# Kernel tuning notes

Hardware: AMD Instinct MI355X
Metric: run time of the kernel (lower is better)

## Reference

```python
import math
import jax, jax.numpy as jnp
import numpy as np

B, N, W, D, H = 16, 64, 128, 128, 4

def posenc(L, d):
    pos = jnp.arange(L, dtype=jnp.float32)[:, None]
    div = jnp.exp(jnp.arange(0, d, 2, dtype=jnp.float32) * (-math.log(10000.0) / d))
    pe = jnp.zeros((L, d), jnp.float32)
    pe = pe.at[:, 0::2].set(jnp.sin(pos * div))
    pe = pe.at[:, 1::2].set(jnp.cos(pos * div))
    return pe

def ln(x):
    # torch nn.LayerNorm(x.shape[1:]) created fresh each call: normalize over all non-batch dims, no affine
    ax = tuple(range(1, x.ndim))
    m = x.mean(ax, keepdims=True)
    v = ((x - m) ** 2).mean(ax, keepdims=True)
    return (x - m) / jnp.sqrt(v + 1e-5)

def conv1d(x, w, b):
    # x [B,C,L], w [Cout,Cin,K] (torch layout), VALID padding
    y = jax.lax.conv_general_dilated(x, w, (1,), 'VALID', dimension_numbers=('NCH', 'OIH', 'NCH'))
    return y + b[None, :, None]

def convt1d(x, w, b, stride, pad):
    # torch ConvTranspose1d, w [Cin,Cout,K]
    K = w.shape[2]
    w_ = jnp.flip(w, 2).transpose(1, 0, 2)  # [Cout,Cin,K]
    y = jax.lax.conv_general_dilated(x, w_, (1,), [(K - 1 - pad, K - 1 - pad)],
                                     lhs_dilation=(stride,), dimension_numbers=('NCH', 'OIH', 'NCH'))
    return y + b[None, :, None]

def mha(q, k, v, wi, bi, wo, bo):
    # torch nn.MultiheadAttention(batch_first=True), H heads
    d = q.shape[-1]
    qp = q @ wi[:d].T + bi[:d]
    kp = k @ wi[d:2 * d].T + bi[d:2 * d]
    vp = v @ wi[2 * d:].T + bi[2 * d:]
    def heads(t):
        b_, l_, _ = t.shape
        return t.reshape(b_, l_, H, d // H).transpose(0, 2, 1, 3)
    qh, kh, vh = heads(qp), heads(kp), heads(vp)
    s = jnp.einsum('bhqd,bhkd->bhqk', qh, kh) / jnp.sqrt(jnp.asarray(d // H, qh.dtype))
    o = jnp.einsum('bhqk,bhkd->bhqd', jax.nn.softmax(s, -1), vh)
    b_, l_ = q.shape[0], q.shape[1]
    return o.transpose(0, 2, 1, 3).reshape(b_, l_, d) @ wo.T + bo


def setup_inputs():
    key = jax.random.key(0)
    ks = iter(jax.random.split(key, 64))
    def w(shape, s=0.05):
        return jax.random.normal(next(ks), shape, jnp.float32) * s
    inp = {}
    inp['tokens'] = jax.random.randint(next(ks), (B, N, W), 0, 257, jnp.int32)
    inp['emb_table'] = w((257, D), 1.0)
    for nm in ['ce', 'ct', 'cg', 'ces', 'cts']:
        inp['w_' + nm] = w((D, D, 3))
        inp['b_' + nm] = w((D,))
    inp['mha_wi'] = w((3 * D, D)); inp['mha_bi'] = w((3 * D,))
    inp['mha_wo'] = w((D, D)); inp['mha_bo'] = w((D,))
    s = 1.0 / math.sqrt(D)
    inp['tgt1'] = jax.random.uniform(next(ks), (1, D), jnp.float32, -s, s)
    inp['tgt2'] = jax.random.uniform(next(ks), (1, D), jnp.float32, -s, s)
    for nm in ['mu', 'lv', 'di']:
        inp['w_' + nm] = w((D, D)); inp['b_' + nm] = w((D,))
    inp['eps'] = jax.random.normal(next(ks), (B, D), jnp.float32)
    inp['dk_w'] = w((32, 32)); inp['dk_b'] = w((32,))
    inp['dv_w'] = w((32, 32)); inp['dv_b'] = w((32,))
    inp['wt1'] = w((32, 64, 3)); inp['bt1'] = w((64,))
    inp['wt2'] = w((64, 128, 3)); inp['bt2'] = w((128,))
    for nm in ['sq', 'sk', 'sv']:
        inp[nm + '_w'] = w((128, 128)); inp[nm + '_b'] = w((128,))
    inp['wt3'] = w((128, 128, 3)); inp['bt3'] = w((128,))
    return inp


def reference(tokens, emb_table, w_ce, b_ce, w_ct, b_ct, w_cg, b_cg, w_ces, b_ces, w_cts, b_cts,
              mha_wi, mha_bi, mha_wo, mha_bo, tgt1, tgt2,
              w_mu, b_mu, w_lv, b_lv, w_di, b_di, eps,
              dk_w, dk_b, dv_w, dv_b, wt1, bt1, wt2, bt2,
              sq_w, sq_b, sk_w, sk_b, sv_w, sv_b, wt3, bt3):
    emb = emb_table[tokens] + posenc(W, D)                    # [B,N,W,D]
    flat = emb.reshape(B * N, W, D)                           # batch the per-sample torch loop

    def word_branch(wc, bc, act):
        h = act(conv1d(flat.transpose(0, 2, 1), wc, bc)).transpose(0, 2, 1)  # [BN,W-2,D]
        return mha(h, h, h, mha_wi, mha_bi, mha_wo, mha_bo)

    a_e = jax.nn.elu(word_branch(w_ce, b_ce, jax.nn.elu))
    a_t = jnp.tanh(word_branch(w_ct, b_ct, jnp.tanh))
    xw = ln((a_e * a_t).reshape(B, N, W - 2, D)).reshape(B * N, W - 2, D)

    h = jax.nn.elu(conv1d(xw.transpose(0, 2, 1), w_cg, b_cg)).transpose(0, 2, 1)  # [BN,W-4,D]
    q1 = jnp.broadcast_to(tgt1[None], (B * N, 1, D))
    out = mha(q1, h, h, mha_wi, mha_bi, mha_wo, mha_bo)[:, 0, :].reshape(B, N, D)

    se = out + posenc(N, D)                                   # sentence level

    def sent_branch(wc, bc, act):
        hh = act(conv1d(se.transpose(0, 2, 1), wc, bc)).transpose(0, 2, 1)       # [B,N-2,D]
        return mha(hh, hh, hh, mha_wi, mha_bi, mha_wo, mha_bo)

    s_e = jax.nn.elu(sent_branch(w_ces, b_ces, jax.nn.elu))
    s_t = jnp.tanh(sent_branch(w_cts, b_cts, jnp.tanh))
    xs = ln(s_e * s_t)
    q2 = jnp.broadcast_to(tgt2[None], (B, 1, D))
    doc = mha(q2, xs, xs, mha_wi, mha_bi, mha_wo, mha_bo)[:, 0, :]

    mu = doc @ w_mu.T + b_mu
    lv = doc @ w_lv.T + b_lv
    z = mu + eps * jnp.exp(0.5 * lv)

    h = (z @ w_di.T + b_di).reshape(B, 32, -1)                # [B,32,4]
    L = h.shape[2]
    k = jnp.einsum('oi,bil->bol', dk_w, h) + dk_b[None, :, None]
    v = jnp.einsum('oi,bil->bol', dv_w, h) + dv_b[None, :, None]
    kh = k.reshape(B, H, 8, L)
    vh = v.reshape(B, H, 8, L)
    att = jax.nn.softmax(jnp.einsum('bhdl,bhdm->bhlm', kh, vh) / jnp.sqrt(8.0), -1)
    h = jax.nn.elu(jnp.einsum('bhlm,bhdm->bhld', att, vh).reshape(B, 32, L))
    h = jax.nn.elu(ln(convt1d(h, wt1, bt1, 2, 1)))            # [B,64,7]
    h = jax.nn.elu(ln(convt1d(h, wt2, bt2, 2, 1)))            # [B,128,13]
    L2 = h.shape[2]
    qc = jnp.einsum('oi,bil->bol', sq_w, h) + sq_b[None, :, None]
    kc = jnp.einsum('oi,bil->bol', sk_w, h) + sk_b[None, :, None]
    vc = jnp.einsum('oi,bil->bol', sv_w, h) + sv_b[None, :, None]
    qh = qc.reshape(B, H, 32, L2)
    khh = kc.reshape(B, H, 32, L2)
    att = jax.nn.softmax(jnp.einsum('bhdl,bhdm->bhlm', qh, khh) / jnp.sqrt(32.0), -1)
    vr = vc.reshape(B, H, 32, L2).reshape(B, H, L2, 32)       # faithful torch .view reinterpretation
    h = jax.nn.elu(jnp.einsum('bhlm,bhmd->bhld', att, vr).reshape(B, 128, L2))
    recon = jax.nn.sigmoid(ln(convt1d(h, wt3, bt3, 1, 1)))    # [B,128,13]
    return recon, mu, lv
```

## Files before the change

kernel.cpp:

```cpp
#include <hip/hip_runtime.h>
#include <hip/hip_bf16.h>

typedef __hip_bfloat16 bf16;
typedef __attribute__((ext_vector_type(8))) short bf16x8;
typedef __attribute__((ext_vector_type(4))) float f32x4;

__device__ __forceinline__ float b2f(bf16 x){ return __bfloat162float(x); }
__device__ __forceinline__ bf16  f2b(float x){ return __float2bfloat16(x); }

#define LOG2E 1.4426950408889634f

__device__ __forceinline__ float fexp2(float x){
  float r; asm("v_exp_f32 %0, %1" : "=v"(r) : "v"(x)); return r;
}
__device__ __forceinline__ float fast_exp(float x){ return fexp2(x * LOG2E); }
__device__ __forceinline__ float eluf(float x){ return x > 0.f ? x : fast_exp(x) - 1.f; }
__device__ __forceinline__ float fast_tanh(float x){
  float cx = fminf(fmaxf(x, -15.f), 15.f);
  float t = fexp2(cx * (2.f*LOG2E));
  return (t - 1.f) / (t + 1.f);
}

#define PE_C (-0.07195578415606394f)

__device__ __forceinline__ float pe_val(int pos, int d){
  int j2 = d & ~1;
  float ang = (float)pos * expf((float)j2 * PE_C);
  return (d & 1) ? cosf(ang) : sinf(ang);
}

__device__ __forceinline__ void pack_one(const float* __restrict__ W, bf16* __restrict__ out,
                                         int K, int N, int conv, int t){
  int j = t & 7, lane = (t >> 3) & 63;
  int rest = t >> 9; int NT = N >> 4;
  int nt = rest % NT; int kb = rest / NT;
  int k = kb*32 + ((lane >> 4) << 3) + j;
  int n = nt*16 + (lane & 15);
  float v = conv ? W[n*384 + (k & 127)*3 + (k >> 7)] : W[(long)n*K + k];
  out[t] = f2b(v);
}

__global__ void k_prep(const float* __restrict__ w_ce, const float* __restrict__ w_ct,
                       const float* __restrict__ w_cg, const float* __restrict__ w_ces,
                       const float* __restrict__ w_cts, const float* __restrict__ wi,
                       const float* __restrict__ wo,
                       bf16* P_CE, bf16* P_CT, bf16* P_CG, bf16* P_CES, bf16* P_CTS,
                       bf16* P_WI, bf16* P_WO, float* __restrict__ pet){
  int bid = blockIdx.x;
  if (bid < 1152){
    int grp = bid / 192; int t = (bid % 192)*256 + threadIdx.x;
    const float* W; bf16* out; int K, N, conv;
    if      (grp == 0){ W = w_ce;  out = P_CE;  K=384; N=128; conv=1; }
    else if (grp == 1){ W = w_ct;  out = P_CT;  K=384; N=128; conv=1; }
    else if (grp == 2){ W = w_cg;  out = P_CG;  K=384; N=128; conv=1; }
    else if (grp == 3){ W = w_ces; out = P_CES; K=384; N=128; conv=1; }
    else if (grp == 4){ W = w_cts; out = P_CTS; K=384; N=128; conv=1; }
    else              { W = wi;    out = P_WI;  K=128; N=384; conv=0; }
    pack_one(W, out, K, N, conv, t);
  } else if (bid < 1216){
    int t = (bid - 1152)*256 + threadIdx.x;
    pack_one(wo, P_WO, 128, 128, 0, t);
  } else {
    int i = (bid - 1216)*256 + threadIdx.x;
    if (i < 16384) pet[i] = pe_val(i >> 7, i & 127);
  }
}

__global__ void k_qprep(const float* __restrict__ wi, const float* __restrict__ bi,
                        const float* __restrict__ t1, const float* __restrict__ t2,
                        float* __restrict__ rkv){
  int tid = threadIdx.x;
  __shared__ float qps[256];
  {
    int which = tid >> 7, jj = tid & 127;
    const float* t = which ? t2 : t1;
    float a = bi[jj];
    for (int i = 0; i < 128; ++i) a += wi[jj*128 + i] * t[i];
    qps[tid] = a;
  }
  __syncthreads();
  int i = tid & 127, which = tid >> 7;
  for (int h = 0; h < 4; ++h){
    float a = 0.f;
    for (int d = 0; d < 32; ++d) a += qps[which*128 + h*32 + d] * wi[(128 + h*32 + d)*128 + i];
    rkv[which*512 + h*128 + i] = a;
  }
}

__global__ void k_embed8(const int* __restrict__ tok, const float* __restrict__ tab,
                         const float* __restrict__ pet, bf16* __restrict__ out){
  int t = blockIdx.x*256 + threadIdx.x;
  int q = t & 15;
  int flat = t >> 4; int w = flat & 127;
  int tk = tok[flat];
  const float* ta = tab + tk*128 + q*8;
  const float* pe = pet + (w << 7) + q*8;
  bf16 ob[8];
  #pragma unroll
  for (int i = 0; i < 8; ++i) ob[i] = f2b(ta[i] + pe[i]);
  *(f32x4*)(out + (size_t)t*8) = *(f32x4*)ob;
}

__global__ void k_se(const bf16* __restrict__ in, const float* __restrict__ pet, bf16* __restrict__ out){
  int idx = blockIdx.x*256 + threadIdx.x;
  int d = idx & 127; int n = (idx >> 7) & 63;
  out[idx] = f2b(b2f(in[idx]) + pet[(n << 7) + d]);
}

__global__ __launch_bounds__(256)
void k_gemm_mfma(const bf16* __restrict__ A, const bf16* __restrict__ Bp,
                 const float* __restrict__ bias, bf16* __restrict__ C,
                 const bf16* __restrict__ mul,
                 int M, int K, int a_lout, int a_lind, int lda,
                 int NT, int n0t, int ldc, int act,
                 const float* __restrict__ lnst, int lngrp){
  __shared__ f32x4 AsV[2][512];
  char* As0 = (char*)AsV[0];
  char* As1 = (char*)AsV[1];
  int tid = threadIdx.x;
  int lane = tid & 63, wave = tid >> 6;
  int wm = wave >> 1, wn = wave & 1;
  int m0 = blockIdx.x*128;
  int by = blockIdx.y;

  long offA[2]; bool okA[2]; float lnm[2], lnr[2]; int sbyte[2];
  #pragma unroll
  for (int p = 0; p < 2; ++p){
    int e = tid + p*256;
    int row = e >> 2, kq = e & 3, m = m0 + row;
    okA[p] = (m < M);
    long off = 0;
    if (okA[p]){
      off = (a_lout > 0) ? (long)(m / a_lout)*a_lind + (long)(m % a_lout)*128 + kq*8
                         : (long)m*lda + kq*8;
    }
    offA[p] = off;
    lnm[p] = 0.f; lnr[p] = 1.f;
    if (lnst && okA[p]){ int g = (int)(off / (long)lngrp); lnm[p] = lnst[2*g]; lnr[p] = lnst[2*g+1]; }
    sbyte[p] = (row*64 + kq*16) ^ ((row & 7) << 4);
  }
  auto loadA = [&](int p, int kb)->float4{
    float4 v = make_float4(0.f,0.f,0.f,0.f);
    if (okA[p]){
      v = *(const float4*)(A + offA[p] + kb*32);
      if (lnst){
        bf16* pp = (bf16*)&v; bf16 oo[8];
        #pragma unroll
        for (int u = 0; u < 8; ++u) oo[u] = f2b((b2f(pp[u]) - lnm[p]) * lnr[p]);
        v = *(float4*)&oo[0];
      }
    }
    return v;
  };

  const bf16* bptr[4];
  size_t bstep = (size_t)NT*512;
  #pragma unroll
  for (int fn = 0; fn < 4; ++fn){
    int ntile = n0t + by*8 + wn*4 + fn;
    bptr[fn] = Bp + ((size_t)ntile*64 + lane)*8;
  }
  int abyte[4];
  #pragma unroll
  for (int fm = 0; fm < 4; ++fm){
    int row = wm*64 + fm*16 + (lane & 15);
    abyte[fm] = (row*64 + ((lane >> 4) << 4)) ^ ((row & 7) << 4);
  }

  f32x4 acc[4][4];
  #pragma unroll
  for (int i = 0; i < 4; ++i)
    #pragma unroll
    for (int j = 0; j < 4; ++j) acc[i][j] = (f32x4){0.f,0.f,0.f,0.f};

  float4 va0 = loadA(0, 0), va1 = loadA(1, 0);
  *(float4*)(As0 + sbyte[0]) = va0;
  *(float4*)(As0 + sbyte[1]) = va1;
  __syncthreads();

  int nk = K >> 5;
  for (int kb = 0; kb < nk; ++kb){
    char* cur = (kb & 1) ? As1 : As0;
    char* nxt = (kb & 1) ? As0 : As1;
    bool more = (kb + 1) < nk;
    if (more){ va0 = loadA(0, kb+1); va1 = loadA(1, kb+1); }
    bf16x8 bfr[4];
    #pragma unroll
    for (int fn = 0; fn < 4; ++fn) bfr[fn] = *(const bf16x8*)(bptr[fn] + (size_t)kb*bstep);
    bf16x8 afr[4];
    #pragma unroll
    for (int fm = 0; fm < 4; ++fm) afr[fm] = *(const bf16x8*)(cur + abyte[fm]);
    #pragma unroll
    for (int fm = 0; fm < 4; ++fm)
      #pragma unroll
      for (int fn = 0; fn < 4; ++fn)
        acc[fm][fn] = __builtin_amdgcn_mfma_f32_16x16x32_bf16(afr[fm], bfr[fn], acc[fm][fn], 0, 0, 0);
    if (more){
      *(float4*)(nxt + sbyte[0]) = va0;
      *(float4*)(nxt + sbyte[1]) = va1;
    }
    __syncthreads();
  }

  #pragma unroll
  for (int fm = 0; fm < 4; ++fm){
    #pragma unroll
    for (int r = 0; r < 4; ++r){
      int m = m0 + wm*64 + fm*16 + ((lane >> 4) << 2) + r;
      if (m >= M) continue;
      #pragma unroll
      for (int fn = 0; fn < 4; ++fn){
        int n = by*128 + wn*64 + fn*16 + (lane & 15);
        float v = acc[fm][fn][r] + (bias ? bias[n] : 0.f);
        if (act == 1) v = eluf(v);
        else if (act == 2) v = fast_tanh(v);
        if (mul) v *= b2f(mul[(long)m*ldc + n]);
        C[(long)m*ldc + n] = f2b(v);
      }
    }
  }
}

template<int L>
__global__ __launch_bounds__(256)
void k_attn_fused(const bf16* __restrict__ X, const bf16* __restrict__ Pwi,
                  const float* __restrict__ bi, bf16* __restrict__ o){
  constexpr int KB  = (L + 31) / 32;
  constexpr int MT  = KB * 2;
  constexpr int WMT = MT / 4;
  constexpr int NP  = KB * 32;
  constexpr int PRS = NP * 2;

  __shared__ alignas(16) char As[NP*256];
  __shared__ alignas(16) char Qb[NP*64];
  __shared__ alignas(16) char Kb[NP*64];
  __shared__ alignas(16) char Vt[32*PRS];
  char* Pb = As;

  int tid = threadIdx.x;
  int s = blockIdx.x >> 2, h = blockIdx.x & 3;
  const bf16* xb = X + (size_t)s*L*128;

  for (int e = tid; e < NP*16; e += 256){
    int row = e >> 4, c = e & 15;
    float4 v = make_float4(0.f,0.f,0.f,0.f);
    if (row < L) v = *(const float4*)(xb + (size_t)row*128 + c*8);
    *(float4*)(As + ((row*256 + c*16) ^ ((row & 7) << 4))) = v;
  }
  __syncthreads();

  int lane = tid & 63, wave = tid >> 6;
  const float qsc = 0.17677669529663687f * LOG2E;

  __builtin_amdgcn_s_setprio(1);
  #pragma unroll
  for (int mt = 0; mt < WMT; ++mt){
    int mtile = wave*WMT + mt;
    int arow = mtile*16 + (lane & 15);
    bf16x8 a4[4];
    #pragma unroll
    for (int kb = 0; kb < 4; ++kb)
      a4[kb] = *(const bf16x8*)(As + ((arow*256 + kb*64 + ((lane >> 4) << 4)) ^ ((arow & 7) << 4)));
    #pragma unroll
    for (int out = 0; out < 6; ++out){
      int which = out >> 1, nt = out & 1;
      int ntile = which*8 + h*2 + nt;
      f32x4 acc = (f32x4){0.f,0.f,0.f,0.f};
      #pragma unroll
      for (int kb = 0; kb < 4; ++kb){
        bf16x8 bfr = *(const bf16x8*)(Pwi + (((size_t)kb*24 + ntile)*64 + lane)*8);
        acc = __builtin_amdgcn_mfma_f32_16x16x32_bf16(a4[kb], bfr, acc, 0, 0, 0);
      }
      int col = lane & 15;
      float bia = bi[which*128 + h*32 + nt*16 + col];
      #pragma unroll
      for (int r = 0; r < 4; ++r){
        int row = mtile*16 + ((lane >> 4) << 2) + r;
        float outv = acc[r] + bia;
        if (which == 0){
          *(bf16*)(Qb + ((row*64 + (nt*16 + col)*2) ^ ((row & 7) << 4))) = f2b(outv * qsc);
        } else if (which == 1){
          *(bf16*)(Kb + ((row*64 + (nt*16 + col)*2) ^ ((row & 7) << 4))) = f2b(outv);
        } else {
          int d = nt*16 + col;
          *(bf16*)(Vt + ((d*PRS + row*2) ^ ((d & 7) << 4))) = f2b(outv);
        }
      }
    }
  }
  __builtin_amdgcn_s_setprio(0);
  __syncthreads();

  f32x4 acc[WMT][MT];
  #pragma unroll
  for (int mt = 0; mt < WMT; ++mt)
    #pragma unroll
    for (int nt = 0; nt < MT; ++nt) acc[mt][nt] = (f32x4){0.f,0.f,0.f,0.f};

  bf16x8 af[WMT];
  #pragma unroll
  for (int mt = 0; mt < WMT; ++mt){
    int row = (wave*WMT + mt)*16 + (lane & 15);
    af[mt] = *(const bf16x8*)(Qb + ((row*64 + ((lane >> 4) << 4)) ^ ((row & 7) << 4)));
  }
  __builtin_amdgcn_s_setprio(1);
  #pragma unroll
  for (int nt = 0; nt < MT; ++nt){
    int rk2 = nt*16 + (lane & 15);
    bf16x8 bfk = *(const bf16x8*)(Kb + ((rk2*64 + ((lane >> 4) << 4)) ^ ((rk2 & 7) << 4)));
    #pragma unroll
    for (int mt = 0; mt < WMT; ++mt)
      acc[mt][nt] = __builtin_amdgcn_mfma_f32_16x16x32_bf16(af[mt], bfk, acc[mt][nt], 0, 0, 0);
  }
  __builtin_amdgcn_s_setprio(0);

  const bool lastMask = (lane & 15) >= (L - (MT-1)*16);
  float pinv[WMT][4];
  #pragma unroll
  for (int mt = 0; mt < WMT; ++mt){
    #pragma unroll
    for (int r = 0; r < 4; ++r){
      float mx = -1e30f;
      #pragma unroll
      for (int nt = 0; nt < MT; ++nt){
        float v = acc[mt][nt][r];
        if (nt == MT-1 && lastMask){ v = -1e30f; acc[mt][nt][r] = v; }
        mx = fmaxf(mx, v);
      }
      mx = fmaxf(mx, __shfl_xor(mx, 1));
      mx = fmaxf(mx, __shfl_xor(mx, 2));
      mx = fmaxf(mx, __shfl_xor(mx, 4));
      mx = fmaxf(mx, __shfl_xor(mx, 8));
      float sum = 0.f;
      #pragma unroll
      for (int nt = 0; nt < MT; ++nt){
        float p = fexp2(acc[mt][nt][r] - mx);
        acc[mt][nt][r] = p;
        sum += p;
      }
      sum += __shfl_xor(sum, 1);
      sum += __shfl_xor(sum, 2);
      sum += __shfl_xor(sum, 4);
      sum += __shfl_xor(sum, 8);
      pinv[mt][r] = 1.f / sum;
      int row = (wave*WMT + mt)*16 + ((lane >> 4) << 2) + r;
      #pragma unroll
      for (int nt = 0; nt < MT; ++nt){
        int col = nt*16 + (lane & 15);
        *(bf16*)(Pb + ((row*PRS + col*2) ^ ((row & 7) << 4))) = f2b(acc[mt][nt][r]);
      }
    }
  }

  #pragma unroll
  for (int mt = 0; mt < WMT; ++mt){
    int mtile = wave*WMT + mt;
    f32x4 o0 = (f32x4){0.f,0.f,0.f,0.f}, o1 = (f32x4){0.f,0.f,0.f,0.f};
    __builtin_amdgcn_s_setprio(1);
    #pragma unroll
    for (int kb = 0; kb < KB; ++kb){
      int row = mtile*16 + (lane & 15);
      bf16x8 pa = *(const bf16x8*)(Pb + ((row*PRS + kb*64 + ((lane >> 4) << 4)) ^ ((row & 7) << 4)));
      int d0 = lane & 15;
      bf16x8 v0 = *(const bf16x8*)(Vt + ((d0*PRS + kb*64 + ((lane >> 4) << 4)) ^ ((d0 & 7) << 4)));
      bf16x8 v1 = *(const bf16x8*)(Vt + (((d0+16)*PRS + kb*64 + ((lane >> 4) << 4)) ^ (((d0+16) & 7) << 4)));
      o0 = __builtin_amdgcn_mfma_f32_16x16x32_bf16(pa, v0, o0, 0, 0, 0);
      o1 = __builtin_amdgcn_mfma_f32_16x16x32_bf16(pa, v1, o1, 0, 0, 0);
    }
    __builtin_amdgcn_s_setprio(0);
    #pragma unroll
    for (int r = 0; r < 4; ++r){
      int row = mtile*16 + ((lane >> 4) << 2) + r;
      if (row < L){
        size_t ob = ((size_t)s*L + row)*128 + h*32 + (lane & 15);
        o[ob]      = f2b(o0[r] * pinv[mt][r]);
        o[ob + 16] = f2b(o1[r] * pinv[mt][r]);
      }
    }
  }
}

template<int L>
__global__ __launch_bounds__(256)
void k_attn_tgt(const bf16* __restrict__ hin, const float* __restrict__ rk,
                const float* __restrict__ wi, const float* __restrict__ bi,
                bf16* __restrict__ outp){
  __shared__ alignas(16) char Hs[L*256];
  __shared__ float RKs[512];
  __shared__ float Ps[512];
  __shared__ float Cs[512];
  int tid = threadIdx.x, lane = tid & 63, wave = tid >> 6;
  int s = blockIdx.x;
  const bf16* hb = hin + (size_t)s*L*128;
  for (int e = tid; e < L*16; e += 256){
    int row = e >> 4, c = e & 15;
    *(float4*)(Hs + row*256 + ((c ^ (row & 7)) << 4)) = *(const float4*)(hb + row*128 + c*8);
  }
  for (int e = tid; e < 512; e += 256) RKs[e] = rk[e];
  __syncthreads();

  int j0 = lane, j1 = lane + 64;
  float v0 = -1e30f, v1 = -1e30f;
  if (j0 < L){
    float a = 0.f;
    #pragma unroll
    for (int c = 0; c < 16; ++c){
      bf16x8 x = *(const bf16x8*)(Hs + j0*256 + ((c ^ (j0 & 7)) << 4));
      #pragma unroll
      for (int u = 0; u < 8; ++u) a += b2f(((bf16*)&x)[u]) * RKs[wave*128 + c*8 + u];
    }
    v0 = a * 0.17677669529663687f;
  }
  if (j1 < L){
    float a = 0.f;
    #pragma unroll
    for (int c = 0; c < 16; ++c){
      bf16x8 x = *(const bf16x8*)(Hs + j1*256 + ((c ^ (j1 & 7)) << 4));
      #pragma unroll
      for (int u = 0; u < 8; ++u) a += b2f(((bf16*)&x)[u]) * RKs[wave*128 + c*8 + u];
    }
    v1 = a * 0.17677669529663687f;
  }
  float mx = fmaxf(v0, v1);
  #pragma unroll
  for (int off = 32; off; off >>= 1) mx = fmaxf(mx, __shfl_xor(mx, off));
  float e0 = (j0 < L) ? fast_exp(v0 - mx) : 0.f;
  float e1 = (j1 < L) ? fast_exp(v1 - mx) : 0.f;
  float sum = e0 + e1;
  #pragma unroll
  for (int off = 32; off; off >>= 1) sum += __shfl_xor(sum, off);
  float inv = 1.f / sum;
  Ps[wave*128 + j0] = e0 * inv;
  Ps[wave*128 + j1] = e1 * inv;

  int i0 = lane*2;
  float c0 = 0.f, c1 = 0.f;
  for (int j = 0; j < L; ++j){
    float p = Ps[wave*128 + j];
    short2 w2 = *(const short2*)(Hs + j*256 + (((i0 >> 3) ^ (j & 7)) << 4) + (i0 & 7)*2);
    c0 += p * b2f(*(bf16*)&w2.x);
    c1 += p * b2f(*(bf16*)&w2.y);
  }
  Cs[wave*128 + i0]     = c0;
  Cs[wave*128 + i0 + 1] = c1;
  __syncthreads();

  if (tid < 128){
    int h2 = tid >> 5;
    float a = bi[256 + tid];
    const float* wr = wi + (size_t)(256 + tid)*128;
    for (int i = 0; i < 128; ++i) a += wr[i] * Cs[h2*128 + i];
    outp[(size_t)s*128 + tid] = f2b(a);
  }
}

__global__ void k_ln_partial(const bf16* __restrict__ x, float* __restrict__ part, int GS, int P){
  int pi = blockIdx.x % P;
  int chunk8 = GS / P / 8;
  size_t base = (size_t)(blockIdx.x / P)*GS + (size_t)pi*(GS/P);
  float s = 0.f, s2 = 0.f;
  for (int i = threadIdx.x; i < chunk8; i += 256){
    f32x4 raw = *(const f32x4*)(x + base + (size_t)i*8);
    const bf16* xb = (const bf16*)&raw;
    #pragma unroll
    for (int j = 0; j < 8; ++j){ float v = b2f(xb[j]); s += v; s2 += v*v; }
  }
  #pragma unroll
  for (int off = 32; off; off >>= 1){ s += __shfl_xor(s, off); s2 += __shfl_xor(s2, off); }
  __shared__ float sh[8];
  int lane = threadIdx.x & 63, wv = threadIdx.x >> 6;
  if (lane == 0){ sh[wv] = s; sh[4 + wv] = s2; }
  __syncthreads();
  if (threadIdx.x == 0){
    part[blockIdx.x*2]     = sh[0]+sh[1]+sh[2]+sh[3];
    part[blockIdx.x*2 + 1] = sh[4]+sh[5]+sh[6]+sh[7];
  }
}

__global__ void k_ln_fin(const float* __restrict__ part, float* __restrict__ stats, int P, int GS){
  int g = blockIdx.x;
  float s = 0.f, s2 = 0.f;
  for (int i = threadIdx.x; i < P; i += 256){ s += part[(g*P + i)*2]; s2 += part[(g*P + i)*2 + 1]; }
  #pragma unroll
  for (int off = 32; off; off >>= 1){ s += __shfl_xor(s, off); s2 += __shfl_xor(s2, off); }
  __shared__ float sh[8];
  int lane = threadIdx.x & 63, wv = threadIdx.x >> 6;
  if (lane == 0){ sh[wv] = s; sh[4 + wv] = s2; }
  __syncthreads();
  if (threadIdx.x == 0){
    float S = sh[0]+sh[1]+sh[2]+sh[3], S2 = sh[4]+sh[5]+sh[6]+sh[7];
    float mean = S / GS;
    float var = S2 / GS - mean*mean;
    stats[g*2] = mean; stats[g*2 + 1] = rsqrtf(var + 1e-5f);
  }
}

__global__ void k_ln_small_bf16(const bf16* __restrict__ x, bf16* __restrict__ y, int n){
  int g = blockIdx.x;
  const bf16* xb = x + (size_t)g*n;
  bf16* yb = y + (size_t)g*n;
  float s = 0.f, s2 = 0.f;
  for (int i = threadIdx.x; i < n; i += 256){ float v = b2f(xb[i]); s += v; s2 += v*v; }
  #pragma unroll
  for (int off = 32; off; off >>= 1){ s += __shfl_xor(s, off); s2 += __shfl_xor(s2, off); }
  __shared__ float sh[8];  __shared__ float ms[2];
  int lane = threadIdx.x & 63, wv = threadIdx.x >> 6;
  if (lane == 0){ sh[wv] = s; sh[4 + wv] = s2; }
  __syncthreads();
  if (threadIdx.x == 0){
    float S = sh[0]+sh[1]+sh[2]+sh[3], S2 = sh[4]+sh[5]+sh[6]+sh[7];
    float mean = S / n;
    ms[0] = mean; ms[1] = rsqrtf(S2 / n - mean*mean + 1e-5f);
  }
  __syncthreads();
  float mean = ms[0], inv = ms[1];
  for (int i = threadIdx.x; i < n; i += 256) yb[i] = f2b((b2f(xb[i]) - mean)*inv);
}

__global__ void k_ln_small_f32(const float* __restrict__ x, float* __restrict__ y, int n, int act){
  int g = blockIdx.x;
  const float* xb = x + (size_t)g*n;
  float* yb = y + (size_t)g*n;
  float s = 0.f, s2 = 0.f;
  for (int i = threadIdx.x; i < n; i += 256){ float v = xb[i]; s += v; s2 += v*v; }
  #pragma unroll
  for (int off = 32; off; off >>= 1){ s += __shfl_xor(s, off); s2 += __shfl_xor(s2, off); }
  __shared__ float sh[8];  __shared__ float ms[2];
  int lane = threadIdx.x & 63, wv = threadIdx.x >> 6;
  if (lane == 0){ sh[wv] = s; sh[4 + wv] = s2; }
  __syncthreads();
  if (threadIdx.x == 0){
    float S = sh[0]+sh[1]+sh[2]+sh[3], S2 = sh[4]+sh[5]+sh[6]+sh[7];
    float mean = S / n;
    ms[0] = mean; ms[1] = rsqrtf(S2 / n - mean*mean + 1e-5f);
  }
  __syncthreads();
  float mean = ms[0], inv = ms[1];
  for (int i = threadIdx.x; i < n; i += 256){
    float v = (xb[i] - mean)*inv;
    if (act == 1) v = eluf(v);
    else if (act == 3) v = 1.f/(1.f + fast_exp(-v));
    yb[i] = v;
  }
}

__global__ void k_muz(const bf16* __restrict__ doc, const float* __restrict__ w_mu, const float* __restrict__ b_mu,
                      const float* __restrict__ w_lv, const float* __restrict__ b_lv,
                      const float* __restrict__ eps, float* __restrict__ mu_out, float* __restrict__ lv_out,
                      float* __restrict__ z){
  int t = blockIdx.x*256 + threadIdx.x;
  if (t >= 2048) return;
  int b = t >> 7, j = t & 127;
  const bf16* dr = doc + b*128;
  float mu = b_mu[j], lv = b_lv[j];
  for (int i = 0; i < 128; ++i){
    float x = b2f(dr[i]);
    mu += x * w_mu[j*128 + i];
    lv += x * w_lv[j*128 + i];
  }
  mu_out[t] = mu; lv_out[t] = lv;
  z[t] = mu + eps[t] * fast_exp(0.5f * lv);
}

__global__ void k_vecmat(const float* __restrict__ x, const float* __restrict__ w,
                         const float* __restrict__ bias, float* __restrict__ y){
  int t = blockIdx.x*256 + threadIdx.x;
  if (t >= 2048) return;
  int b = t >> 7, j = t & 127;
  float a = bias[j];
  const float* xb = x + b*128;
  for (int i = 0; i < 128; ++i) a += xb[i] * w[j*128 + i];
  y[t] = a;
}

__global__ void k_chanproj2(const float* __restrict__ x,
                            const float* __restrict__ w1, const float* __restrict__ b1,
                            const float* __restrict__ w2, const float* __restrict__ b2,
                            float* __restrict__ y1, float* __restrict__ y2,
                            int Bn, int C, int L){
  int idx = blockIdx.x*256 + threadIdx.x;
  if (idx >= Bn*C*L) return;
  int l = idx % L; int t2 = idx / L; int o = t2 % C; int b = t2 / C;
  float a1 = b1[o], a2 = b2[o];
  const float* xb = x + (size_t)b*C*L + l;
  for (int i = 0; i < C; ++i){
    float xv = xb[i*L];
    a1 += w1[(size_t)o*C + i]*xv;
    a2 += w2[(size_t)o*C + i]*xv;
  }
  y1[idx] = a1; y2[idx] = a2;
}

__global__ void k_chanproj3(const float* __restrict__ x,
                            const float* __restrict__ w1, const float* __restrict__ b1,
                            const float* __restrict__ w2, const float* __restrict__ b2,
                            const float* __restrict__ w3, const float* __restrict__ b3,
                            float* __restrict__ y1, float* __restrict__ y2, float* __restrict__ y3,
                            int Bn, int C, int L){
  int idx = blockIdx.x*256 + threadIdx.x;
  if (idx >= Bn*C*L) return;
  int l = idx % L; int t2 = idx / L; int o = t2 % C; int b = t2 / C;
  float a1 = b1[o], a2 = b2[o], a3 = b3[o];
  const float* xb = x + (size_t)b*C*L + l;
  for (int i = 0; i < C; ++i){
    float xv = xb[i*L];
    a1 += w1[(size_t)o*C + i]*xv;
    a2 += w2[(size_t)o*C + i]*xv;
    a3 += w3[(size_t)o*C + i]*xv;
  }
  y1[idx] = a1; y2[idx] = a2; y3[idx] = a3;
}

__global__ __launch_bounds__(128)
void k_dec_attn1(const float* __restrict__ kd, const float* __restrict__ vd, float* __restrict__ out){
  int b = blockIdx.x, tid = threadIdx.x;
  __shared__ float ksh[128], vsh[128], sc[64];
  ksh[tid] = kd[b*128 + tid]; vsh[tid] = vd[b*128 + tid];
  __syncthreads();
  if (tid < 64){
    int h = tid >> 4, l = (tid >> 2) & 3, m = tid & 3;
    float a = 0.f;
    #pragma unroll
    for (int d = 0; d < 8; ++d) a += ksh[(h*8 + d)*4 + l] * vsh[(h*8 + d)*4 + m];
    sc[tid] = a * 0.35355339059327373f;
  }
  __syncthreads();
  if (tid < 16){
    int base = tid*4;
    float mx = fmaxf(fmaxf(sc[base], sc[base+1]), fmaxf(sc[base+2], sc[base+3]));
    float e0 = fast_exp(sc[base]-mx), e1 = fast_exp(sc[base+1]-mx), e2 = fast_exp(sc[base+2]-mx), e3 = fast_exp(sc[base+3]-mx);
    float inv = 1.f/(e0+e1+e2+e3);
    sc[base] = e0*inv; sc[base+1] = e1*inv; sc[base+2] = e2*inv; sc[base+3] = e3*inv;
  }
  __syncthreads();
  {
    int h = tid >> 5, rem = tid & 31, l = rem >> 3, d = rem & 7;
    float a = 0.f;
    #pragma unroll
    for (int m = 0; m < 4; ++m) a += sc[h*16 + l*4 + m] * vsh[(h*8 + d)*4 + m];
    out[b*128 + tid] = eluf(a);
  }
}

__global__ __launch_bounds__(256)
void k_dec_attn2(const float* __restrict__ qc, const float* __restrict__ kc,
                 const float* __restrict__ vc, float* __restrict__ out){
  int b = blockIdx.x >> 2, h = blockIdx.x & 3, tid = threadIdx.x;
  __shared__ float sc[169];
  const float* qb = qc + b*1664 + h*416;
  const float* kb = kc + b*1664 + h*416;
  const float* vb = vc + b*1664 + h*416;
  if (tid < 169){
    int l = tid/13, m = tid - l*13;
    float a = 0.f;
    #pragma unroll
    for (int d = 0; d < 32; ++d) a += qb[d*13 + l] * kb[d*13 + m];
    sc[tid] = a * 0.17677669529663687f;
  }
  __syncthreads();
  if (tid < 13){
    float mx = -1e30f;
    for (int m = 0; m < 13; ++m) mx = fmaxf(mx, sc[tid*13 + m]);
    float s = 0.f;
    for (int m = 0; m < 13; ++m){ float p = fast_exp(sc[tid*13 + m] - mx); sc[tid*13 + m] = p; s += p; }
    float inv = 1.f/s;
    for (int m = 0; m < 13; ++m) sc[tid*13 + m] *= inv;
  }
  __syncthreads();
  for (int idx = tid; idx < 416; idx += 256){
    int l = idx >> 5, d = idx & 31;
    float a = 0.f;
    for (int m = 0; m < 13; ++m) a += sc[l*13 + m] * vb[m*32 + d];
    out[b*1664 + h*416 + idx] = eluf(a);
  }
}

__global__ __launch_bounds__(256)
void k_convt(const float* __restrict__ x, const float* __restrict__ w,
             const float* __restrict__ bias, float* __restrict__ y,
             int Bn, int Ci, int Co, int Lin, int Lout, int stride, int pad, int nch){
  __shared__ float xs[1664];
  int b = blockIdx.x / nch;
  int c0 = (blockIdx.x % nch)*16;
  int tid = threadIdx.x;
  for (int i = tid; i < Ci*Lin; i += 256) xs[i] = x[(size_t)b*Ci*Lin + i];
  __syncthreads();
  int co = c0 + (tid & 15);
  int lo = tid >> 4;
  if (co >= Co || lo >= Lout) return;
  float a = bias[co];
  for (int k = 0; k < 3; ++k){
    int t = lo + pad - k;
    if (t < 0 || (t % stride)) continue;
    int li = t / stride;
    if (li >= Lin) continue;
    float aa = 0.f;
    for (int ci = 0; ci < Ci; ++ci) aa += xs[ci*Lin + li] * w[(size_t)ci*Co*3 + co*3 + k];
    a += aa;
  }
  y[(size_t)b*Co*Lout + co*Lout + lo] = a;
}

extern "C" void kernel_launch(void* const* d_in, const int* in_sizes, int n_in,
                              void* d_out, int out_size, void* d_ws, size_t ws_size,
                              hipStream_t stream){
  const int*   tokens = (const int*)  d_in[0];
  const float* tab    = (const float*)d_in[1];
  const float* w_ce = (const float*)d_in[2];  const float* b_ce = (const float*)d_in[3];
  const float* w_ct = (const float*)d_in[4];  const float* b_ct = (const float*)d_in[5];
  const float* w_cg = (const float*)d_in[6];  const float* b_cg = (const float*)d_in[7];
  const float* w_ces= (const float*)d_in[8];  const float* b_ces= (const float*)d_in[9];
  const float* w_cts= (const float*)d_in[10]; const float* b_cts= (const float*)d_in[11];
  const float* wi   = (const float*)d_in[12]; const float* bi   = (const float*)d_in[13];
  const float* wo   = (const float*)d_in[14]; const float* bo   = (const float*)d_in[15];
  const float* tgt1 = (const float*)d_in[16]; const float* tgt2 = (const float*)d_in[17];
  const float* w_mu = (const float*)d_in[18]; const float* b_mu = (const float*)d_in[19];
  const float* w_lv = (const float*)d_in[20]; const float* b_lv = (const float*)d_in[21];
  const float* w_di = (const float*)d_in[22]; const float* b_di = (const float*)d_in[23];
  const float* epsb = (const float*)d_in[24];
  const float* dk_w = (const float*)d_in[25]; const float* dk_b = (const float*)d_in[26];
  const float* dv_w = (const float*)d_in[27]; const float* dv_b = (const float*)d_in[28];
  const float* wt1  = (const float*)d_in[29]; const float* bt1  = (const float*)d_in[30];
  const float* wt2  = (const float*)d_in[31]; const float* bt2  = (const float*)d_in[32];
  const float* sq_w = (const float*)d_in[33]; const float* sq_b = (const float*)d_in[34];
  const float* sk_w = (const float*)d_in[35]; const float* sk_b = (const float*)d_in[36];
  const float* sv_w = (const float*)d_in[37]; const float* sv_b = (const float*)d_in[38];
  const float* wt3  = (const float*)d_in[39]; const float* bt3  = (const float*)d_in[40];

  float* dout = (float*)d_out;

  char* ws = (char*)d_ws;
  size_t off = 0;
  auto take = [&](size_t bytes)->char*{ char* p = ws + off; off += (bytes + 255) & ~(size_t)255; return p; };
  bf16* EMB  = (bf16*)take(16777216ull*2);
  bf16* HB   = (bf16*)take(16515072ull*2);
  bf16* OB   = (bf16*)take(16515072ull*2);
  bf16* AE   = (bf16*)take(16515072ull*2);
  bf16* O1   = (bf16*)take(131072ull*2);
  bf16* OUTB = (bf16*)take(131072ull*2);
  bf16* SEB  = (bf16*)take(131072ull*2);
  bf16* SH   = (bf16*)take(126976ull*2);
  bf16* SCT  = (bf16*)take(126976ull*2);
  bf16* SO   = (bf16*)take(126976ull*2);
  bf16* SAE  = (bf16*)take(126976ull*2);
  bf16* XS   = (bf16*)take(126976ull*2);
  bf16* DO1  = (bf16*)take(2048ull*2);
  bf16* DOC  = (bf16*)take(2048ull*2);
  float* RK  = (float*)take(1024*4);
  float* PART= (float*)take(2016ull*2*4);
  float* STATS=(float*)take(32*4);
  float* Z   = (float*)take(2048*4);
  float* H3  = (float*)take(2048*4);
  float* KD  = (float*)take(2048*4);
  float* VD  = (float*)take(2048*4);
  float* DEC1= (float*)take(2048*4);
  float* C1  = (float*)take(7168*4);
  float* DEC2= (float*)take(7168*4);
  float* C2  = (float*)take(26624*4);
  float* DEC3= (float*)take(26624*4);
  float* QC  = (float*)take(26624*4);
  float* KC  = (float*)take(26624*4);
  float* VC  = (float*)take(26624*4);
  float* DEC4= (float*)take(26624*4);
  float* C3  = (float*)take(26624*4);
  float* PET = (float*)take(16384*4);
  bf16* P_CE = (bf16*)take(49152ull*2);
  bf16* P_CT = (bf16*)take(49152ull*2);
  bf16* P_CG = (bf16*)take(49152ull*2);
  bf16* P_CES= (bf16*)take(49152ull*2);
  bf16* P_CTS= (bf16*)take(49152ull*2);
  bf16* P_WI = (bf16*)take(49152ull*2);
  bf16* P_WO = (bf16*)take(16384ull*2);
  (void)ws_size; (void)in_sizes; (void)n_in; (void)out_size;

  auto cdiv = [](long a, long b){ return (int)((a + b - 1)/b); };
  auto gemm = [&](const bf16* A, const bf16* Bpp, const float* bias, bf16* C, const bf16* mul,
                  int M, int N, int K, int a_lout, int a_lind, int lda, int NT, int n0t, int ldc, int act,
                  const float* lnst, int lngrp){
    dim3 g(cdiv(M,128), N/128);
    k_gemm_mfma<<<g, 256, 0, stream>>>(A, Bpp, bias, C, mul,
                                       M, K, a_lout, a_lind, lda, NT, n0t, ldc, act, lnst, lngrp);
  };

  k_prep<<<1280, 256, 0, stream>>>(w_ce, w_ct, w_cg, w_ces, w_cts, wi, wo,
                                   P_CE, P_CT, P_CG, P_CES, P_CTS, P_WI, P_WO, PET);
  k_qprep<<<1, 256, 0, stream>>>(wi, bi, tgt1, tgt2, RK);
  k_embed8<<<8192, 256, 0, stream>>>(tokens, tab, PET, EMB);

  gemm(EMB, P_CE, b_ce, HB, nullptr, 129024, 128, 384, 126, 16384, 0, 8, 0, 128, 1, nullptr, 0);
  gemm(EMB, P_CT, b_ct, OB, nullptr, 129024, 128, 384, 126, 16384, 0, 8, 0, 128, 2, nullptr, 0);

  k_attn_fused<126><<<4096, 256, 0, stream>>>(HB, P_WI, bi, EMB);
  gemm(EMB, P_WO, bo, AE, nullptr, 129024, 128, 128, 0, 0, 128, 8, 0, 128, 1, nullptr, 0);

  k_attn_fused<126><<<4096, 256, 0, stream>>>(OB, P_WI, bi, EMB);
  gemm(EMB, P_WO, bo, HB, AE, 129024, 128, 128, 0, 0, 128, 8, 0, 128, 2, nullptr, 0);

  k_ln_partial<<<2016, 256, 0, stream>>>(HB, PART, 1032192, 126);
  k_ln_fin<<<16, 256, 0, stream>>>(PART, STATS, 126, 1032192);

  gemm(HB, P_CG, b_cg, OB, nullptr, 126976, 128, 384, 124, 16128, 0, 8, 0, 128, 1, STATS, 1032192);

  k_attn_tgt<124><<<1024, 256, 0, stream>>>(OB, RK, wi, bi, O1);
  gemm(O1, P_WO, bo, OUTB, nullptr, 1024, 128, 128, 0, 0, 128, 8, 0, 128, 0, nullptr, 0);

  k_se<<<512, 256, 0, stream>>>(OUTB, PET, SEB);

  gemm(SEB, P_CES, b_ces, SH, nullptr, 992, 128, 384, 62, 8192, 0, 8, 0, 128, 1, nullptr, 0);
  gemm(SEB, P_CTS, b_cts, SCT, nullptr, 992, 128, 384, 62, 8192, 0, 8, 0, 128, 2, nullptr, 0);

  k_attn_fused<62><<<64, 256, 0, stream>>>(SH, P_WI, bi, SO);
  gemm(SO, P_WO, bo, SAE, nullptr, 992, 128, 128, 0, 0, 128, 8, 0, 128, 1, nullptr, 0);

  k_attn_fused<62><<<64, 256, 0, stream>>>(SCT, P_WI, bi, SO);
  gemm(SO, P_WO, bo, SH, SAE, 992, 128, 128, 0, 0, 128, 8, 0, 128, 2, nullptr, 0);

  k_ln_small_bf16<<<16, 256, 0, stream>>>(SH, XS, 7936);

  k_attn_tgt<62><<<16, 256, 0, stream>>>(XS, RK + 512, wi, bi, DO1);
  gemm(DO1, P_WO, bo, DOC, nullptr, 16, 128, 128, 0, 0, 128, 8, 0, 128, 0, nullptr, 0);

  k_muz<<<8, 256, 0, stream>>>(DOC, w_mu, b_mu, w_lv, b_lv, epsb, dout + 26624, dout + 28672, Z);
  k_vecmat<<<8, 256, 0, stream>>>(Z, w_di, b_di, H3);
  k_chanproj2<<<8, 256, 0, stream>>>(H3, dk_w, dk_b, dv_w, dv_b, KD, VD, 16, 32, 4);
  k_dec_attn1<<<16, 128, 0, stream>>>(KD, VD, DEC1);
  k_convt<<<16*4, 256, 0, stream>>>(DEC1, wt1, bt1, C1, 16, 32, 64, 4, 7, 2, 1, 4);
  k_ln_small_f32<<<16, 256, 0, stream>>>(C1, DEC2, 448, 1);
  k_convt<<<16*8, 256, 0, stream>>>(DEC2, wt2, bt2, C2, 16, 64, 128, 7, 13, 2, 1, 8);
  k_ln_small_f32<<<16, 256, 0, stream>>>(C2, DEC3, 1664, 1);
  k_chanproj3<<<cdiv(26624,256), 256, 0, stream>>>(DEC3, sq_w, sq_b, sk_w, sk_b, sv_w, sv_b,
                                                   QC, KC, VC, 16, 128, 13);
  k_dec_attn2<<<64, 256, 0, stream>>>(QC, KC, VC, DEC4);
  k_convt<<<16*8, 256, 0, stream>>>(DEC4, wt3, bt3, C3, 16, 128, 128, 13, 13, 1, 1, 8);
  k_ln_small_f32<<<16, 256, 0, stream>>>(C3, dout, 1664, 3);
}
```

Measured before the change: 724.0 us.

## Fuse decoder into one kernel, batch paired GEMMs, fold Q scale into weights

Twelve small decoder kernels become a single per-batch kernel that keeps intermediates in shared memory. Paired conv GEMMs that share an input now run as one launch using blockIdx.z to select weights, bias and output. The attention Q scale moves into the packed weights, and the attention kernel writes Q/K and P to shared memory as packed bf16 words instead of single halves. This cuts launch overhead and LDS store count, but the fused decoder runs only 16 blocks serially through its stages, and the V row permutation in LDS must stay consistent with how it is read.

```diff
diff --git a/kernel.cpp b/kernel.cpp
--- a/kernel.cpp
+++ b/kernel.cpp
@@ -7,8 +7,10 @@
 
 __device__ __forceinline__ float b2f(bf16 x){ return __bfloat162float(x); }
 __device__ __forceinline__ bf16  f2b(float x){ return __float2bfloat16(x); }
+__device__ __forceinline__ unsigned short b2u(bf16 x){ union{bf16 b; unsigned short u;} c; c.b = x; return c.u; }
 
 #define LOG2E 1.4426950408889634f
+#define QSC (0.17677669529663687f * LOG2E)
 
 __device__ __forceinline__ float fexp2(float x){
   float r; asm("v_exp_f32 %0, %1" : "=v"(r) : "v"(x)); return r;
@@ -30,13 +32,14 @@
 }
 
 __device__ __forceinline__ void pack_one(const float* __restrict__ W, bf16* __restrict__ out,
-                                         int K, int N, int conv, int t){
+                                         int K, int N, int conv, int qscale, int t){
   int j = t & 7, lane = (t >> 3) & 63;
   int rest = t >> 9; int NT = N >> 4;
   int nt = rest % NT; int kb = rest / NT;
   int k = kb*32 + ((lane >> 4) << 3) + j;
   int n = nt*16 + (lane & 15);
   float v = conv ? W[n*384 + (k & 127)*3 + (k >> 7)] : W[(long)n*K + k];
+  if (qscale && n < 128) v *= QSC;
   out[t] = f2b(v);
 }
 
@@ -49,17 +52,17 @@
   int bid = blockIdx.x;
   if (bid < 1152){
     int grp = bid / 192; int t = (bid % 192)*256 + threadIdx.x;
-    const float* W; bf16* out; int K, N, conv;
+    const float* W; bf16* out; int K, N, conv, qs = 0;
     if      (grp == 0){ W = w_ce;  out = P_CE;  K=384; N=128; conv=1; }
     else if (grp == 1){ W = w_ct;  out = P_CT;  K=384; N=128; conv=1; }
     else if (grp == 2){ W = w_cg;  out = P_CG;  K=384; N=128; conv=1; }
     else if (grp == 3){ W = w_ces; out = P_CES; K=384; N=128; conv=1; }
     else if (grp == 4){ W = w_cts; out = P_CTS; K=384; N=128; conv=1; }
-    else              { W = wi;    out = P_WI;  K=128; N=384; conv=0; }
-    pack_one(W, out, K, N, conv, t);
+    else              { W = wi;    out = P_WI;  K=128; N=384; conv=0; qs=1; }
+    pack_one(W, out, K, N, conv, qs, t);
   } else if (bid < 1216){
     int t = (bid - 1152)*256 + threadIdx.x;
-    pack_one(wo, P_WO, 128, 128, 0, t);
+    pack_one(wo, P_WO, 128, 128, 0, 0, t);
   } else {
     int i = (bid - 1216)*256 + threadIdx.x;
     if (i < 16384) pet[i] = pe_val(i >> 7, i & 127);
@@ -108,12 +111,16 @@
 }
 
 __global__ __launch_bounds__(256)
-void k_gemm_mfma(const bf16* __restrict__ A, const bf16* __restrict__ Bp,
-                 const float* __restrict__ bias, bf16* __restrict__ C,
+void k_gemm_mfma(const bf16* __restrict__ A, const bf16* __restrict__ Bp_, const bf16* __restrict__ Bp2,
+                 const float* __restrict__ bias_, const float* __restrict__ bias2,
+                 bf16* __restrict__ C_, bf16* __restrict__ C2p,
                  const bf16* __restrict__ mul,
                  int M, int K, int a_lout, int a_lind, int lda,
-                 int NT, int n0t, int ldc, int act,
+                 int NT, int n0t, int ldc, int act_, int act2,
                  const float* __restrict__ lnst, int lngrp){
+  const bf16* Bp = Bp_; const float* bias = bias_; bf16* C = C_; int act = act_;
+  if (blockIdx.z){ Bp = Bp2; bias = bias2; C = C2p; act = act2; }
+
   __shared__ f32x4 AsV[2][512];
   char* As0 = (char*)AsV[0];
   char* As1 = (char*)AsV[1];
@@ -250,40 +257,46 @@
   __syncthreads();
 
   int lane = tid & 63, wave = tid >> 6;
-  const float qsc = 0.17677669529663687f * LOG2E;
+  int col = lane & 15;
 
   __builtin_amdgcn_s_setprio(1);
   #pragma unroll
   for (int mt = 0; mt < WMT; ++mt){
     int mtile = wave*WMT + mt;
-    int arow = mtile*16 + (lane & 15);
+    int arow = mtile*16 + col;
     bf16x8 a4[4];
     #pragma unroll
     for (int kb = 0; kb < 4; ++kb)
       a4[kb] = *(const bf16x8*)(As + ((arow*256 + kb*64 + ((lane >> 4) << 4)) ^ ((arow & 7) << 4)));
     #pragma unroll
-    for (int out = 0; out < 6; ++out){
-      int which = out >> 1, nt = out & 1;
-      int ntile = which*8 + h*2 + nt;
-      f32x4 acc = (f32x4){0.f,0.f,0.f,0.f};
+    for (int which = 0; which < 3; ++which){
+      f32x4 av[2];
       #pragma unroll
-      for (int kb = 0; kb < 4; ++kb){
-        bf16x8 bfr = *(const bf16x8*)(Pwi + (((size_t)kb*24 + ntile)*64 + lane)*8);
-        acc = __builtin_amdgcn_mfma_f32_16x16x32_bf16(a4[kb], bfr, acc, 0, 0, 0);
+      for (int nt = 0; nt < 2; ++nt){
+        int ntile = which*8 + h*2 + nt;
+        float bia = bi[which*128 + h*32 + nt*16 + col];
+        if (which == 0) bia *= QSC;
+        av[nt] = (f32x4){bia, bia, bia, bia};
+        #pragma unroll
+        for (int kb = 0; kb < 4; ++kb){
+          bf16x8 bfr = *(const bf16x8*)(Pwi + (((size_t)kb*24 + ntile)*64 + lane)*8);
+          av[nt] = __builtin_amdgcn_mfma_f32_16x16x32_bf16(a4[kb], bfr, av[nt], 0, 0, 0);
+        }
       }
-      int col = lane & 15;
-      float bia = bi[which*128 + h*32 + nt*16 + col];
       #pragma unroll
       for (int r = 0; r < 4; ++r){
         int row = mtile*16 + ((lane >> 4) << 2) + r;
-        float outv = acc[r] + bia;
-        if (which == 0){
-          *(bf16*)(Qb + ((row*64 + (nt*16 + col)*2) ^ ((row & 7) << 4))) = f2b(outv * qsc);
-        } else if (which == 1){
-          *(bf16*)(Kb + ((row*64 + (nt*16 + col)*2) ^ ((row & 7) << 4))) = f2b(outv);
+        if (which < 2){
+          unsigned pk = (unsigned)b2u(f2b(av[0][r])) | ((unsigned)b2u(f2b(av[1][r])) << 16);
+          char* dst = which ? Kb : Qb;
+          *(unsigned*)(dst + ((row*64 + col*4) ^ ((row & 7) << 4))) = pk;
         } else {
-          int d = nt*16 + col;
-          *(bf16*)(Vt + ((d*PRS + row*2) ^ ((d & 7) << 4))) = f2b(outv);
+          int pos = (row & 15)*MT + (row >> 4);
+          #pragma unroll
+          for (int nt = 0; nt < 2; ++nt){
+            int d = nt*16 + col;
+            *(bf16*)(Vt + ((d*PRS + pos*2) ^ ((d & 7) << 4))) = f2b(av[nt][r]);
+          }
         }
       }
     }
@@ -300,13 +313,13 @@
   bf16x8 af[WMT];
   #pragma unroll
   for (int mt = 0; mt < WMT; ++mt){
-    int row = (wave*WMT + mt)*16 + (lane & 15);
+    int row = (wave*WMT + mt)*16 + col;
     af[mt] = *(const bf16x8*)(Qb + ((row*64 + ((lane >> 4) << 4)) ^ ((row & 7) << 4)));
   }
   __builtin_amdgcn_s_setprio(1);
   #pragma unroll
   for (int nt = 0; nt < MT; ++nt){
-    int rk2 = nt*16 + (lane & 15);
+    int rk2 = nt*16 + col;
     bf16x8 bfk = *(const bf16x8*)(Kb + ((rk2*64 + ((lane >> 4) << 4)) ^ ((rk2 & 7) << 4)));
     #pragma unroll
     for (int mt = 0; mt < WMT; ++mt)
@@ -314,7 +327,7 @@
   }
   __builtin_amdgcn_s_setprio(0);
 
-  const bool lastMask = (lane & 15) >= (L - (MT-1)*16);
+  const bool lastMask = col >= (L - (MT-1)*16);
   float pinv[WMT][4];
   #pragma unroll
   for (int mt = 0; mt < WMT; ++mt){
@@ -332,10 +345,11 @@
       mx = fmaxf(mx, __shfl_xor(mx, 4));
       mx = fmaxf(mx, __shfl_xor(mx, 8));
       float sum = 0.f;
+      bf16 prow[MT];
       #pragma unroll
       for (int nt = 0; nt < MT; ++nt){
         float p = fexp2(acc[mt][nt][r] - mx);
-        acc[mt][nt][r] = p;
+        prow[nt] = f2b(p);
         sum += p;
       }
       sum += __shfl_xor(sum, 1);
@@ -344,11 +358,9 @@
       sum += __shfl_xor(sum, 8);
       pinv[mt][r] = 1.f / sum;
       int row = (wave*WMT + mt)*16 + ((lane >> 4) << 2) + r;
-      #pragma unroll
-      for (int nt = 0; nt < MT; ++nt){
-        int col = nt*16 + (lane & 15);
-        *(bf16*)(Pb + ((row*PRS + col*2) ^ ((row & 7) << 4))) = f2b(acc[mt][nt][r]);
-      }
+      char* dst = Pb + ((row*PRS + col*(MT*2)) ^ ((row & 7) << 4));
+      if constexpr (MT == 8) *(f32x4*)dst = *(f32x4*)prow;
+      else                   *(float2*)dst = *(float2*)prow;
     }
   }
 
@@ -359,9 +371,9 @@
     __builtin_amdgcn_s_setprio(1);
     #pragma unroll
     for (int kb = 0; kb < KB; ++kb){
-      int row = mtile*16 + (lane & 15);
+      int row = mtile*16 + col;
       bf16x8 pa = *(const bf16x8*)(Pb + ((row*PRS + kb*64 + ((lane >> 4) << 4)) ^ ((row & 7) << 4)));
-      int d0 = lane & 15;
+      int d0 = col;
       bf16x8 v0 = *(const bf16x8*)(Vt + ((d0*PRS + kb*64 + ((lane >> 4) << 4)) ^ ((d0 & 7) << 4)));
       bf16x8 v1 = *(const bf16x8*)(Vt + (((d0+16)*PRS + kb*64 + ((lane >> 4) << 4)) ^ (((d0+16) & 7) << 4)));
       o0 = __builtin_amdgcn_mfma_f32_16x16x32_bf16(pa, v0, o0, 0, 0, 0);
@@ -372,7 +384,7 @@
     for (int r = 0; r < 4; ++r){
       int row = mtile*16 + ((lane >> 4) << 2) + r;
       if (row < L){
-        size_t ob = ((size_t)s*L + row)*128 + h*32 + (lane & 15);
+        size_t ob = ((size_t)s*L + row)*128 + h*32 + col;
         o[ob]      = f2b(o0[r] * pinv[mt][r]);
         o[ob + 16] = f2b(o1[r] * pinv[mt][r]);
       }
@@ -517,188 +529,191 @@
   for (int i = threadIdx.x; i < n; i += 256) yb[i] = f2b((b2f(xb[i]) - mean)*inv);
 }
 
-__global__ void k_ln_small_f32(const float* __restrict__ x, float* __restrict__ y, int n, int act){
-  int g = blockIdx.x;
-  const float* xb = x + (size_t)g*n;
-  float* yb = y + (size_t)g*n;
-  float s = 0.f, s2 = 0.f;
-  for (int i = threadIdx.x; i < n; i += 256){ float v = xb[i]; s += v; s2 += v*v; }
-  #pragma unroll
-  for (int off = 32; off; off >>= 1){ s += __shfl_xor(s, off); s2 += __shfl_xor(s2, off); }
-  __shared__ float sh[8];  __shared__ float ms[2];
-  int lane = threadIdx.x & 63, wv = threadIdx.x >> 6;
-  if (lane == 0){ sh[wv] = s; sh[4 + wv] = s2; }
-  __syncthreads();
-  if (threadIdx.x == 0){
-    float S = sh[0]+sh[1]+sh[2]+sh[3], S2 = sh[4]+sh[5]+sh[6]+sh[7];
-    float mean = S / n;
-    ms[0] = mean; ms[1] = rsqrtf(S2 / n - mean*mean + 1e-5f);
-  }
-  __syncthreads();
-  float mean = ms[0], inv = ms[1];
-  for (int i = threadIdx.x; i < n; i += 256){
-    float v = (xb[i] - mean)*inv;
-    if (act == 1) v = eluf(v);
-    else if (act == 3) v = 1.f/(1.f + fast_exp(-v));
-    yb[i] = v;
-  }
-}
-
-__global__ void k_muz(const bf16* __restrict__ doc, const float* __restrict__ w_mu, const float* __restrict__ b_mu,
-                      const float* __restrict__ w_lv, const float* __restrict__ b_lv,
-                      const float* __restrict__ eps, float* __restrict__ mu_out, float* __restrict__ lv_out,
-                      float* __restrict__ z){
-  int t = blockIdx.x*256 + threadIdx.x;
-  if (t >= 2048) return;
-  int b = t >> 7, j = t & 127;
-  const bf16* dr = doc + b*128;
-  float mu = b_mu[j], lv = b_lv[j];
-  for (int i = 0; i < 128; ++i){
-    float x = b2f(dr[i]);
-    mu += x * w_mu[j*128 + i];
-    lv += x * w_lv[j*128 + i];
-  }
-  mu_out[t] = mu; lv_out[t] = lv;
-  z[t] = mu + eps[t] * fast_exp(0.5f * lv);
-}
-
-__global__ void k_vecmat(const float* __restrict__ x, const float* __restrict__ w,
-                         const float* __restrict__ bias, float* __restrict__ y){
-  int t = blockIdx.x*256 + threadIdx.x;
-  if (t >= 2048) return;
-  int b = t >> 7, j = t & 127;
-  float a = bias[j];
-  const float* xb = x + b*128;
-  for (int i = 0; i < 128; ++i) a += xb[i] * w[j*128 + i];
-  y[t] = a;
-}
-
-__global__ void k_chanproj2(const float* __restrict__ x,
-                            const float* __restrict__ w1, const float* __restrict__ b1,
-                            const float* __restrict__ w2, const float* __restrict__ b2,
-                            float* __restrict__ y1, float* __restrict__ y2,
-                            int Bn, int C, int L){
-  int idx = blockIdx.x*256 + threadIdx.x;
-  if (idx >= Bn*C*L) return;
-  int l = idx % L; int t2 = idx / L; int o = t2 % C; int b = t2 / C;
-  float a1 = b1[o], a2 = b2[o];
-  const float* xb = x + (size_t)b*C*L + l;
-  for (int i = 0; i < C; ++i){
-    float xv = xb[i*L];
-    a1 += w1[(size_t)o*C + i]*xv;
-    a2 += w2[(size_t)o*C + i]*xv;
-  }
-  y1[idx] = a1; y2[idx] = a2;
-}
-
-__global__ void k_chanproj3(const float* __restrict__ x,
-                            const float* __restrict__ w1, const float* __restrict__ b1,
-                            const float* __restrict__ w2, const float* __restrict__ b2,
-                            const float* __restrict__ w3, const float* __restrict__ b3,
-                            float* __restrict__ y1, float* __restrict__ y2, float* __restrict__ y3,
-                            int Bn, int C, int L){
-  int idx = blockIdx.x*256 + threadIdx.x;
-  if (idx >= Bn*C*L) return;
-  int l = idx % L; int t2 = idx / L; int o = t2 % C; int b = t2 / C;
-  float a1 = b1[o], a2 = b2[o], a3 = b3[o];
-  const float* xb = x + (size_t)b*C*L + l;
-  for (int i = 0; i < C; ++i){
-    float xv = xb[i*L];
-    a1 += w1[(size_t)o*C + i]*xv;
-    a2 += w2[(size_t)o*C + i]*xv;
-    a3 += w3[(size_t)o*C + i]*xv;
-  }
-  y1[idx] = a1; y2[idx] = a2; y3[idx] = a3;
-}
-
-__global__ __launch_bounds__(128)
-void k_dec_attn1(const float* __restrict__ kd, const float* __restrict__ vd, float* __restrict__ out){
+__global__ __launch_bounds__(256)
+void k_decoder(const bf16* __restrict__ DOC,
+               const float* __restrict__ w_mu, const float* __restrict__ b_mu,
+               const float* __restrict__ w_lv, const float* __restrict__ b_lv,
+               const float* __restrict__ eps,
+               const float* __restrict__ w_di, const float* __restrict__ b_di,
+               const float* __restrict__ dk_w, const float* __restrict__ dk_b,
+               const float* __restrict__ dv_w, const float* __restrict__ dv_b,
+               const float* __restrict__ wt1, const float* __restrict__ bt1,
+               const float* __restrict__ wt2, const float* __restrict__ bt2,
+               const float* __restrict__ sq_w, const float* __restrict__ sq_b,
+               const float* __restrict__ sk_w, const float* __restrict__ sk_b,
+               const float* __restrict__ sv_w, const float* __restrict__ sv_b,
+               const float* __restrict__ wt3, const float* __restrict__ bt3,
+               float* __restrict__ dout){
   int b = blockIdx.x, tid = threadIdx.x;
-  __shared__ float ksh[128], vsh[128], sc[64];
-  ksh[tid] = kd[b*128 + tid]; vsh[tid] = vd[b*128 + tid];
+  __shared__ float Zs[128], H3[128], KD[128], VD[128], D1[128];
+  __shared__ float C1[448], D2[448];
+  __shared__ float C2a[1664], D3[1664];
+  __shared__ float QC[1664], KC[1664], VC[1664], D4[1664], C3a[1664];
+  __shared__ float sc[676];
+  __shared__ float red[8], ms[2];
+
+  auto lnact = [&](const float* x, float* y, int n, int act){
+    float s = 0.f, s2 = 0.f;
+    for (int i = tid; i < n; i += 256){ float v = x[i]; s += v; s2 += v*v; }
+    #pragma unroll
+    for (int o = 32; o; o >>= 1){ s += __shfl_xor(s, o); s2 += __shfl_xor(s2, o); }
+    int lane = tid & 63, wv = tid >> 6;
+    if (lane == 0){ red[wv] = s; red[4+wv] = s2; }
+    __syncthreads();
+    if (tid == 0){
+      float S = red[0]+red[1]+red[2]+red[3], S2 = red[4]+red[5]+red[6]+red[7];
+      float mean = S/n; ms[0] = mean; ms[1] = rsqrtf(S2/n - mean*mean + 1e-5f);
+    }
+    __syncthreads();
+    float mean = ms[0], inv = ms[1];
+    for (int i = tid; i < n; i += 256){
+      float v = (x[i]-mean)*inv;
+      if (act == 1) v = eluf(v);
+      else if (act == 3) v = 1.f/(1.f + fast_exp(-v));
+      y[i] = v;
+    }
+    __syncthreads();
+  };
+
+  if (tid < 128){
+    const bf16* dr = DOC + b*128;
+    float mu = b_mu[tid], lv = b_lv[tid];
+    for (int i = 0; i < 128; ++i){
+      float x = b2f(dr[i]);
+      mu += x * w_mu[tid*128 + i];
+      lv += x * w_lv[tid*128 + i];
+    }
+    dout[26624 + b*128 + tid] = mu;
+    dout[28672 + b*128 + tid] = lv;
+    Zs[tid] = mu + eps[b*128 + tid] * fast_exp(0.5f*lv);
+  }
+  __syncthreads();
+  if (tid < 128){
+    float a = b_di[tid];
+    for (int i = 0; i < 128; ++i) a += Zs[i] * w_di[tid*128 + i];
+    H3[tid] = a;
+  }
+  __syncthreads();
+  if (tid < 128){
+    int l = tid & 3, o2 = tid >> 2;
+    float ak = dk_b[o2], av = dv_b[o2];
+    for (int i = 0; i < 32; ++i){
+      float xv = H3[i*4 + l];
+      ak += dk_w[o2*32 + i]*xv;
+      av += dv_w[o2*32 + i]*xv;
+    }
+    KD[tid] = ak; VD[tid] = av;
+  }
   __syncthreads();
   if (tid < 64){
     int h = tid >> 4, l = (tid >> 2) & 3, m = tid & 3;
     float a = 0.f;
     #pragma unroll
-    for (int d = 0; d < 8; ++d) a += ksh[(h*8 + d)*4 + l] * vsh[(h*8 + d)*4 + m];
+    for (int d = 0; d < 8; ++d) a += KD[(h*8+d)*4 + l] * VD[(h*8+d)*4 + m];
     sc[tid] = a * 0.35355339059327373f;
   }
   __syncthreads();
   if (tid < 16){
     int base = tid*4;
-    float mx = fmaxf(fmaxf(sc[base], sc[base+1]), fmaxf(sc[base+2], sc[base+3]));
-    float e0 = fast_exp(sc[base]-mx), e1 = fast_exp(sc[base+1]-mx), e2 = fast_exp(sc[base+2]-mx), e3 = fast_exp(sc[base+3]-mx);
+    float mx = fmaxf(fmaxf(sc[base],sc[base+1]),fmaxf(sc[base+2],sc[base+3]));
+    float e0=fast_exp(sc[base]-mx), e1=fast_exp(sc[base+1]-mx), e2=fast_exp(sc[base+2]-mx), e3=fast_exp(sc[base+3]-mx);
     float inv = 1.f/(e0+e1+e2+e3);
-    sc[base] = e0*inv; sc[base+1] = e1*inv; sc[base+2] = e2*inv; sc[base+3] = e3*inv;
-  }
-  __syncthreads();
-  {
+    sc[base]=e0*inv; sc[base+1]=e1*inv; sc[base+2]=e2*inv; sc[base+3]=e3*inv;
+  }
+  __syncthreads();
+  if (tid < 128){
     int h = tid >> 5, rem = tid & 31, l = rem >> 3, d = rem & 7;
     float a = 0.f;
     #pragma unroll
-    for (int m = 0; m < 4; ++m) a += sc[h*16 + l*4 + m] * vsh[(h*8 + d)*4 + m];
-    out[b*128 + tid] = eluf(a);
-  }
-}
-
-__global__ __launch_bounds__(256)
-void k_dec_attn2(const float* __restrict__ qc, const float* __restrict__ kc,
-                 const float* __restrict__ vc, float* __restrict__ out){
-  int b = blockIdx.x >> 2, h = blockIdx.x & 3, tid = threadIdx.x;
-  __shared__ float sc[169];
-  const float* qb = qc + b*1664 + h*416;
-  const float* kb = kc + b*1664 + h*416;
-  const float* vb = vc + b*1664 + h*416;
-  if (tid < 169){
-    int l = tid/13, m = tid - l*13;
+    for (int m = 0; m < 4; ++m) a += sc[h*16 + l*4 + m] * VD[(h*8+d)*4 + m];
+    D1[tid] = eluf(a);
+  }
+  __syncthreads();
+  for (int idx = tid; idx < 448; idx += 256){
+    int co = idx / 7, lo = idx % 7;
+    float a = bt1[co];
+    for (int k = 0; k < 3; ++k){
+      int t = lo + 1 - k;
+      if (t < 0 || (t & 1)) continue;
+      int li = t >> 1; if (li >= 4) continue;
+      float aa = 0.f;
+      for (int ci = 0; ci < 32; ++ci) aa += D1[ci*4 + li] * wt1[ci*192 + co*3 + k];
+      a += aa;
+    }
+    C1[idx] = a;
+  }
+  __syncthreads();
+  lnact(C1, D2, 448, 1);
+  for (int idx = tid; idx < 1664; idx += 256){
+    int co = idx / 13, lo = idx % 13;
+    float a = bt2[co];
+    for (int k = 0; k < 3; ++k){
+      int t = lo + 1 - k;
+      if (t < 0 || (t & 1)) continue;
+      int li = t >> 1; if (li >= 7) continue;
+      float aa = 0.f;
+      for (int ci = 0; ci < 64; ++ci) aa += D2[ci*7 + li] * wt2[ci*384 + co*3 + k];
+      a += aa;
+    }
+    C2a[idx] = a;
+  }
+  __syncthreads();
+  lnact(C2a, D3, 1664, 1);
+  for (int idx = tid; idx < 1664; idx += 256){
+    int o = idx / 13, l = idx % 13;
+    float a1 = sq_b[o], a2 = sk_b[o], a3 = sv_b[o];
+    for (int i = 0; i < 128; ++i){
+      float xv = D3[i*13 + l];
+      a1 += sq_w[o*128 + i]*xv;
+      a2 += sk_w[o*128 + i]*xv;
+      a3 += sv_w[o*128 + i]*xv;
+    }
+    QC[idx] = a1; KC[idx] = a2; VC[idx] = a3;
+  }
+  __syncthreads();
+  for (int idx = tid; idx < 676; idx += 256){
+    int h = idx / 169, rem = idx % 169;
+    int l = rem / 13, m = rem % 13;
     float a = 0.f;
     #pragma unroll
-    for (int d = 0; d < 32; ++d) a += qb[d*13 + l] * kb[d*13 + m];
-    sc[tid] = a * 0.17677669529663687f;
-  }
-  __syncthreads();
-  if (tid < 13){
+    for (int d = 0; d < 32; ++d) a += QC[h*416 + d*13 + l] * KC[h*416 + d*13 + m];
+    sc[idx] = a * 0.17677669529663687f;
+  }
+  __syncthreads();
+  if (tid < 52){
+    int h = tid / 13, l = tid % 13;
+    float* row = sc + h*169 + l*13;
     float mx = -1e30f;
-    for (int m = 0; m < 13; ++m) mx = fmaxf(mx, sc[tid*13 + m]);
-    float s = 0.f;
-    for (int m = 0; m < 13; ++m){ float p = fast_exp(sc[tid*13 + m] - mx); sc[tid*13 + m] = p; s += p; }
-    float inv = 1.f/s;
-    for (int m = 0; m < 13; ++m) sc[tid*13 + m] *= inv;
-  }
-  __syncthreads();
-  for (int idx = tid; idx < 416; idx += 256){
-    int l = idx >> 5, d = idx & 31;
+    for (int m = 0; m < 13; ++m) mx = fmaxf(mx, row[m]);
+    float ssum = 0.f;
+    for (int m = 0; m < 13; ++m){ float p = fast_exp(row[m]-mx); row[m] = p; ssum += p; }
+    float inv = 1.f/ssum;
+    for (int m = 0; m < 13; ++m) row[m] *= inv;
+  }
+  __syncthreads();
+  for (int idx = tid; idx < 1664; idx += 256){
+    int h = idx / 416, rem = idx % 416;
+    int l = rem >> 5, d = rem & 31;
     float a = 0.f;
-    for (int m = 0; m < 13; ++m) a += sc[l*13 + m] * vb[m*32 + d];
-    out[b*1664 + h*416 + idx] = eluf(a);
-  }
-}
-
-__global__ __launch_bounds__(256)
-void k_convt(const float* __restrict__ x, const float* __restrict__ w,
-             const float* __restrict__ bias, float* __restrict__ y,
-             int Bn, int Ci, int Co, int Lin, int Lout, int stride, int pad, int nch){
-  __shared__ float xs[1664];
-  int b = blockIdx.x / nch;
-  int c0 = (blockIdx.x % nch)*16;
-  int tid = threadIdx.x;
-  for (int i = tid; i < Ci*Lin; i += 256) xs[i] = x[(size_t)b*Ci*Lin + i];
-  __syncthreads();
-  int co = c0 + (tid & 15);
-  int lo = tid >> 4;
-  if (co >= Co || lo >= Lout) return;
-  float a = bias[co];
-  for (int k = 0; k < 3; ++k){
-    int t = lo + pad - k;
-    if (t < 0 || (t % stride)) continue;
-    int li = t / stride;
-    if (li >= Lin) continue;
-    float aa = 0.f;
-    for (int ci = 0; ci < Ci; ++ci) aa += xs[ci*Lin + li] * w[(size_t)ci*Co*3 + co*3 + k];
-    a += aa;
-  }
-  y[(size_t)b*Co*Lout + co*Lout + lo] = a;
+    for (int m = 0; m < 13; ++m) a += sc[h*169 + l*13 + m] * VC[h*416 + m*32 + d];
+    D4[idx] = eluf(a);
+  }
+  __syncthreads();
+  for (int idx = tid; idx < 1664; idx += 256){
+    int co = idx / 13, lo = idx % 13;
+    float a = bt3[co];
+    for (int k = 0; k < 3; ++k){
+      int li = lo + 1 - k;
+      if (li < 0 || li >= 13) continue;
+      float aa = 0.f;
+      for (int ci = 0; ci < 128; ++ci) aa += D4[ci*13 + li] * wt3[ci*384 + co*3 + k];
+      a += aa;
+    }
+    C3a[idx] = a;
+  }
+  __syncthreads();
+  lnact(C3a, D4, 1664, 3);
+  for (int i = tid; i < 1664; i += 256) dout[b*1664 + i] = D4[i];
 }
 
 extern "C" void kernel_launch(void* const* d_in, const int* in_sizes, int n_in,
@@ -749,20 +764,6 @@
   float* RK  = (float*)take(1024*4);
   float* PART= (float*)take(2016ull*2*4);
   float* STATS=(float*)take(32*4);
-  float* Z   = (float*)take(2048*4);
-  float* H3  = (float*)take(2048*4);
-  float* KD  = (float*)take(2048*4);
-  float* VD  = (float*)take(2048*4);
-  float* DEC1= (float*)take(2048*4);
-  float* C1  = (float*)take(7168*4);
-  float* DEC2= (float*)take(7168*4);
-  float* C2  = (float*)take(26624*4);
-  float* DEC3= (float*)take(26624*4);
-  float* QC  = (float*)take(26624*4);
-  float* KC  = (float*)take(26624*4);
-  float* VC  = (float*)take(26624*4);
-  float* DEC4= (float*)take(26624*4);
-  float* C3  = (float*)take(26624*4);
   float* PET = (float*)take(16384*4);
   bf16* P_CE = (bf16*)take(49152ull*2);
   bf16* P_CT = (bf16*)take(49152ull*2);
@@ -777,9 +778,16 @@
   auto gemm = [&](const bf16* A, const bf16* Bpp, const float* bias, bf16* C, const bf16* mul,
                   int M, int N, int K, int a_lout, int a_lind, int lda, int NT, int n0t, int ldc, int act,
                   const float* lnst, int lngrp){
-    dim3 g(cdiv(M,128), N/128);
-    k_gemm_mfma<<<g, 256, 0, stream>>>(A, Bpp, bias, C, mul,
-                                       M, K, a_lout, a_lind, lda, NT, n0t, ldc, act, lnst, lngrp);
+    dim3 g(cdiv(M,128), N/128, 1);
+    k_gemm_mfma<<<g, 256, 0, stream>>>(A, Bpp, Bpp, bias, bias, C, C, mul,
+                                       M, K, a_lout, a_lind, lda, NT, n0t, ldc, act, act, lnst, lngrp);
+  };
+  auto gemmz = [&](const bf16* A, const bf16* Bp1, const float* b1, bf16* C1, int act1,
+                   const bf16* Bp2, const float* b2, bf16* C2, int act2,
+                   int M, int N, int K, int a_lout, int a_lind, int lda, int NT, int n0t, int ldc){
+    dim3 g(cdiv(M,128), N/128, 2);
+    k_gemm_mfma<<<g, 256, 0, stream>>>(A, Bp1, Bp2, b1, b2, C1, C2, nullptr,
+                                       M, K, a_lout, a_lind, lda, NT, n0t, ldc, act1, act2, nullptr, 0);
   };
 
   k_prep<<<1280, 256, 0, stream>>>(w_ce, w_ct, w_cg, w_ces, w_cts, wi, wo,
@@ -787,8 +795,7 @@
   k_qprep<<<1, 256, 0, stream>>>(wi, bi, tgt1, tgt2, RK);
   k_embed8<<<8192, 256, 0, stream>>>(tokens, tab, PET, EMB);
 
-  gemm(EMB, P_CE, b_ce, HB, nullptr, 129024, 128, 384, 126, 16384, 0, 8, 0, 128, 1, nullptr, 0);
-  gemm(EMB, P_CT, b_ct, OB, nullptr, 129024, 128, 384, 126, 16384, 0, 8, 0, 128, 2, nullptr, 0);
+  gemmz(EMB, P_CE, b_ce, HB, 1, P_CT, b_ct, OB, 2, 129024, 128, 384, 126, 16384, 0, 8, 0, 128);
 
   k_attn_fused<126><<<4096, 256, 0, stream>>>(HB, P_WI, bi, EMB);
   gemm(EMB, P_WO, bo, AE, nullptr, 129024, 128, 128, 0, 0, 128, 8, 0, 128, 1, nullptr, 0);
@@ -806,8 +813,7 @@
 
   k_se<<<512, 256, 0, stream>>>(OUTB, PET, SEB);
 
-  gemm(SEB, P_CES, b_ces, SH, nullptr, 992, 128, 384, 62, 8192, 0, 8, 0, 128, 1, nullptr, 0);
-  gemm(SEB, P_CTS, b_cts, SCT, nullptr, 992, 128, 384, 62, 8192, 0, 8, 0, 128, 2, nullptr, 0);
+  gemmz(SEB, P_CES, b_ces, SH, 1, P_CTS, b_cts, SCT, 2, 992, 128, 384, 62, 8192, 0, 8, 0, 128);
 
   k_attn_fused<62><<<64, 256, 0, stream>>>(SH, P_WI, bi, SO);
   gemm(SO, P_WO, bo, SAE, nullptr, 992, 128, 128, 0, 0, 128, 8, 0, 128, 1, nullptr, 0);
@@ -820,17 +826,7 @@
   k_attn_tgt<62><<<16, 256, 0, stream>>>(XS, RK + 512, wi, bi, DO1);
   gemm(DO1, P_WO, bo, DOC, nullptr, 16, 128, 128, 0, 0, 128, 8, 0, 128, 0, nullptr, 0);
 
-  k_muz<<<8, 256, 0, stream>>>(DOC, w_mu, b_mu, w_lv, b_lv, epsb, dout + 26624, dout + 28672, Z);
-  k_vecmat<<<8, 256, 0, stream>>>(Z, w_di, b_di, H3);
-  k_chanproj2<<<8, 256, 0, stream>>>(H3, dk_w, dk_b, dv_w, dv_b, KD, VD, 16, 32, 4);
-  k_dec_attn1<<<16, 128, 0, stream>>>(KD, VD, DEC1);
-  k_convt<<<16*4, 256, 0, stream>>>(DEC1, wt1, bt1, C1, 16, 32, 64, 4, 7, 2, 1, 4);
-  k_ln_small_f32<<<16, 256, 0, stream>>>(C1, DEC2, 448, 1);
-  k_convt<<<16*8, 256, 0, stream>>>(DEC2, wt2, bt2, C2, 16, 64, 128, 7, 13, 2, 1, 8);
-  k_ln_small_f32<<<16, 256, 0, stream>>>(C2, DEC3, 1664, 1);
-  k_chanproj3<<<cdiv(26624,256), 256, 0, stream>>>(DEC3, sq_w, sq_b, sk_w, sk_b, sv_w, sv_b,
-                                                   QC, KC, VC, 16, 128, 13);
-  k_dec_attn2<<<64, 256, 0, stream>>>(QC, KC, VC, DEC4);
-  k_convt<<<16*8, 256, 0, stream>>>(DEC4, wt3, bt3, C3, 16, 128, 128, 13, 13, 1, 1, 8);
-  k_ln_small_f32<<<16, 256, 0, stream>>>(C3, dout, 1664, 3);
-}
+  k_decoder<<<16, 256, 0, stream>>>(DOC, w_mu, b_mu, w_lv, b_lv, epsb, w_di, b_di,
+                                    dk_w, dk_b, dv_w, dv_b, wt1, bt1, wt2, bt2,
+                                    sq_w, sq_b, sk_w, sk_b, sv_w, sv_b, wt3, bt3, dout);
+}
```

Result: faster. 701.4 us (-3.1%).
